# Kernel tuning notes

Hardware: AMD Instinct MI355X
Metric: run time of the kernel (lower is better)

## Reference

```python
import jax, jax.numpy as jnp
import numpy as np

N_NEIGHBORS = 5
N_TRAIN = 65536
N_TEST = 4096
DIM = 512
N_CLASSES = 10


def setup_inputs() -> dict:
    key = jax.random.key(0)
    k1, k2, k3 = jax.random.split(key, 3)
    X_train = jax.random.normal(k1, (N_TRAIN, DIM), dtype=jnp.float32)
    X_test = jax.random.normal(k2, (N_TEST, DIM), dtype=jnp.float32)
    y_train = jax.random.randint(k3, (N_TRAIN,), 0, N_CLASSES, dtype=jnp.int64)
    return {"X_train": X_train, "X_test": X_test, "y_train": y_train}


def _knn_predict(X_train, X_test, y_train, k):
    # Euclidean distances via the expanded form (GEMM-dominated):
    # ||t - x||^2 = ||t||^2 + ||x||^2 - 2 t.x
    t2 = jnp.sum(X_test * X_test, axis=-1, keepdims=True)          # [Nt, 1]
    x2 = jnp.sum(X_train * X_train, axis=-1)                        # [Ntr]
    cross = X_test @ X_train.T                                      # [Nt, Ntr]
    d2 = jnp.maximum(t2 + x2[None, :] - 2.0 * cross, 0.0)
    distances = jnp.sqrt(d2)                                        # cdist p=2

    # k smallest distances -> neighbor indices
    _, indices = jax.lax.top_k(-distances, k)                       # [Nt, k]
    nearest = y_train[indices]                                      # [Nt, k]

    counts = jnp.sum(nearest[:, :, None] == nearest[:, None, :], axis=-1)  # [Nt,k,k]->[Nt,k]
    max_c = jnp.max(counts, axis=-1, keepdims=True)
    big = jnp.iinfo(nearest.dtype).max
    candidates = jnp.where(counts == max_c, nearest, big)
    predictions = jnp.min(candidates, axis=-1)                      # [Nt]
    return predictions


def reference(X_train, X_test, y_train):
    return _knn_predict(X_train, X_test, y_train, N_NEIGHBORS)
```

## Files before the change

kernel.cpp:

```cpp
#include <hip/hip_runtime.h>
#include <cstdint>

#define N_TRAIN 65536
#define N_TEST  4096
#define DIM     512
#define K_NN    5
#define NSEG    32
#define SEG     (N_TRAIN / NSEG)

#define GTM 128
#define GTN 128
#define GBK 128
#define NCAND (NSEG * K_NN)
#define NRES  24
#define NSTEP ((SEG / GTN) * (DIM / GBK))
#define KMASK 0xFFFFF800u

typedef float f32x4  __attribute__((ext_vector_type(4)));
typedef float f32x16 __attribute__((ext_vector_type(16)));
typedef int   i32x8  __attribute__((ext_vector_type(8)));

#define GLDS16(g, l)                                                          \
    __builtin_amdgcn_global_load_lds(                                         \
        (__attribute__((address_space(1))) void*)(g),                         \
        (__attribute__((address_space(3))) void*)(l), 16, 0, 0)

__device__ inline unsigned f2e4m3_sw(float x) {
    float ax = fabsf(x);
    unsigned sgn = (__float_as_uint(x) >> 31) << 7;
    if (ax != ax) return sgn | 0x7Fu;
    if (ax >= 448.0f) return sgn | 0x7Eu;
    int ebits = (int)((__float_as_uint(ax) >> 23) & 0xFF);
    int e = ebits - 127;
    int shift = (e < -6 ? -6 : e) - 3;
    float q = exp2f((float)shift);
    float r = rintf(ax / q) * q;
    if (r >= 448.0f) return sgn | 0x7Eu;
    if (r == 0.0f) return sgn;
    unsigned ru = __float_as_uint(r);
    int re = (int)((ru >> 23) & 0xFF) - 127;
    if (re < -6) {
        unsigned k = (unsigned)(r * 512.0f);
        return sgn | k;
    }
    unsigned rm = (ru >> 20) & 0x7u;
    return sgn | ((unsigned)(re + 7) << 3) | rm;
}

__device__ inline unsigned pk4_fp8(float x0, float x1, float x2, float x3) {
#if __has_builtin(__builtin_amdgcn_cvt_pk_fp8_f32)
    unsigned r = (unsigned)__builtin_amdgcn_cvt_pk_fp8_f32(x0, x1, 0, 0);
    r = (unsigned)__builtin_amdgcn_cvt_pk_fp8_f32(x2, x3, (int)r, 1);
    return r;
#else
    return f2e4m3_sw(x0) | (f2e4m3_sw(x1) << 8) |
           (f2e4m3_sw(x2) << 16) | (f2e4m3_sw(x3) << 24);
#endif
}

__global__ __launch_bounds__(256) void cvtnorm8_k(const float* __restrict__ in,
                                                  unsigned char* __restrict__ outb,
                                                  float* __restrict__ outn,
                                                  int nrows) {
    int row  = blockIdx.x * 4 + (threadIdx.x >> 6);
    int lane = threadIdx.x & 63;
    if (row >= nrows) return;
    const float4* p = (const float4*)(in + (size_t)row * DIM) + lane * 2;
    float4 a = p[0], b = p[1];
    float s = a.x*a.x + a.y*a.y + a.z*a.z + a.w*a.w
            + b.x*b.x + b.y*b.y + b.z*b.z + b.w*b.w;
    uint2 v;
    v.x = pk4_fp8(a.x, a.y, a.z, a.w);
    v.y = pk4_fp8(b.x, b.y, b.z, b.w);
    *((uint2*)(outb + (size_t)row * DIM) + lane) = v;
#pragma unroll
    for (int off = 32; off > 0; off >>= 1) s += __shfl_xor(s, off, 64);
    if (lane == 0) outn[row] = s;
}

__global__ __launch_bounds__(256) void norms_k(const float* __restrict__ X,
                                               float* __restrict__ out,
                                               int nrows) {
    int row  = blockIdx.x * 4 + (threadIdx.x >> 6);
    int lane = threadIdx.x & 63;
    if (row >= nrows) return;
    const float4* xp = (const float4*)(X + (size_t)row * DIM);
    float4 a = xp[lane];
    float4 b = xp[lane + 64];
    float s = a.x*a.x + a.y*a.y + a.z*a.z + a.w*a.w
            + b.x*b.x + b.y*b.y + b.z*b.z + b.w*b.w;
#pragma unroll
    for (int off = 32; off > 0; off >>= 1) s += __shfl_down(s, off, 64);
    if (lane == 0) out[row] = s;
}

__device__ inline void ins5(unsigned long long key, unsigned long long* top) {
    if (key < top[4]) {
        unsigned long long k0 = top[0], k1 = top[1], k2 = top[2], k3 = top[3];
        top[0] = key < k0 ? key : k0;
        top[1] = key < k0 ? k0 : (key < k1 ? key : k1);
        top[2] = key < k1 ? k1 : (key < k2 ? key : k2);
        top[3] = key < k2 ? k2 : (key < k3 ? key : k3);
        top[4] = key < k3 ? k3 : key;
    }
}

__device__ inline void ins5u(unsigned key, unsigned* top) {
    if (key < top[4]) {
        unsigned k0 = top[0], k1 = top[1], k2 = top[2], k3 = top[3];
        top[0] = key < k0 ? key : k0;
        top[1] = key < k0 ? k0 : (key < k1 ? key : k1);
        top[2] = key < k1 ? k1 : (key < k2 ? key : k2);
        top[3] = key < k2 ? k2 : (key < k3 ? key : k3);
        top[4] = key < k3 ? k3 : key;
    }
}

__device__ inline unsigned fmono(float v) {
    unsigned u = __float_as_uint(v);
    return (u & 0x80000000u) ? ~u : (u | 0x80000000u);
}

#if __has_builtin(__builtin_amdgcn_mfma_scale_f32_32x32x64_f8f6f4)
__global__ __launch_bounds__(256, 2) void knn_mfma_k(
    const unsigned char* __restrict__ Xtr8,
    const unsigned char* __restrict__ Xte8,
    const float* __restrict__ x2,
    unsigned* __restrict__ cand)
{
    __shared__ __align__(16) unsigned char As[2][GTM * GBK];
    __shared__ __align__(16) unsigned char Bs[2][GTN * GBK];

    const int t    = threadIdx.x;
    const int lane = t & 63;
    const int w    = t >> 6;
    const int wr   = w >> 1, wc = w & 1;
    const int l31  = lane & 31;
    const int hi   = lane >> 5;
    const int r7   = lane & 7;
    const int row0 = blockIdx.x * GTM;
    const int seg0 = blockIdx.y * SEG;

    unsigned top5[2][K_NN];
#pragma unroll
    for (int nt = 0; nt < 2; ++nt)
#pragma unroll
        for (int p = 0; p < K_NN; ++p) top5[nt][p] = 0xFFFFFFFFu;

    int off[4];
#pragma unroll
    for (int j = 0; j < 4; ++j) {
        const int cs = j * 256 + t;
        const int gr = cs >> 3;
        off[j] = gr * DIM + (((cs ^ gr) & 7) << 4);
    }

    auto stage = [&](int s, int b) {
        const int k0 = (s & 3) * GBK;
        const unsigned char* ab = Xte8 + (size_t)row0 * DIM + k0;
        const unsigned char* bb = Xtr8 + (size_t)(seg0 + (s >> 2) * GTN) * DIM + k0;
#pragma unroll
        for (int j = 0; j < 4; ++j) {
            const int ldsb = (j * 256 + w * 64) * 16;
            GLDS16(ab + off[j], &As[b][ldsb]);
            GLDS16(bb + off[j], &Bs[b][ldsb]);
        }
    };

    stage(0, 0);
    __syncthreads();

#pragma unroll 1
    for (int ct = 0; ct < SEG / GTN; ++ct) {
        const int col0 = seg0 + ct * GTN;
        f32x16 acc[2][2];
#pragma unroll
        for (int mt = 0; mt < 2; ++mt)
#pragma unroll
            for (int nt = 0; nt < 2; ++nt)
#pragma unroll
                for (int e = 0; e < 16; ++e) acc[mt][nt][e] = 0.f;

#pragma unroll 1
        for (int kk = 0; kk < DIM / GBK; ++kk) {
            const int s = ct * (DIM / GBK) + kk;
            if (s + 1 < NSTEP) stage(s + 1, (kk + 1) & 1);

            const unsigned char* Ab = As[kk & 1];
            const unsigned char* Bb = Bs[kk & 1];
#pragma unroll
            for (int ks = 0; ks < 2; ++ks) {
                const int xq = (ks * 64 + hi * 32) ^ (r7 << 4);
                i32x8 trf[2], tef[2];
#pragma unroll
                for (int mt = 0; mt < 2; ++mt) {
                    const unsigned char* p = &Bb[(wr * 64 + mt * 32 + l31) * GBK];
                    int4 lo = *(const int4*)&p[xq];
                    int4 hx = *(const int4*)&p[xq ^ 16];
                    trf[mt] = (i32x8){lo.x, lo.y, lo.z, lo.w, hx.x, hx.y, hx.z, hx.w};
                }
#pragma unroll
                for (int nt = 0; nt < 2; ++nt) {
                    const unsigned char* p = &Ab[(wc * 64 + nt * 32 + l31) * GBK];
                    int4 lo = *(const int4*)&p[xq];
                    int4 hx = *(const int4*)&p[xq ^ 16];
                    tef[nt] = (i32x8){lo.x, lo.y, lo.z, lo.w, hx.x, hx.y, hx.z, hx.w};
                }
#pragma unroll
                for (int mt = 0; mt < 2; ++mt)
#pragma unroll
                    for (int nt = 0; nt < 2; ++nt)
                        acc[mt][nt] = __builtin_amdgcn_mfma_scale_f32_32x32x64_f8f6f4(
                            trf[mt], tef[nt], acc[mt][nt],
                            0 , 0 ,
                            0, 0x7F7F7F7F, 0, 0x7F7F7F7F );
            }
            __syncthreads();
        }

        f32x4 x2r[2][4];
#pragma unroll
        for (int mt = 0; mt < 2; ++mt)
#pragma unroll
            for (int g = 0; g < 4; ++g)
                x2r[mt][g] = *(const f32x4*)&x2[col0 + wr * 64 + mt * 32 + g * 8 + 4 * hi];

        const int cbase = ct * GTN + wr * 64;
#pragma unroll
        for (int nt = 0; nt < 2; ++nt) {
            float dv[2][16];
            float gm[2][4];
#pragma unroll
            for (int mt = 0; mt < 2; ++mt)
#pragma unroll
                for (int g = 0; g < 4; ++g) {
#pragma unroll
                    for (int i = 0; i < 4; ++i)
                        dv[mt][g * 4 + i] =
                            fmaf(-2.f, acc[mt][nt][g * 4 + i], x2r[mt][g][i]);
                    gm[mt][g] = fminf(fminf(dv[mt][g*4+0], dv[mt][g*4+1]),
                                      fminf(dv[mt][g*4+2], dv[mt][g*4+3]));
                }
            float dmin = fminf(
                fminf(fminf(gm[0][0], gm[0][1]), fminf(gm[0][2], gm[0][3])),
                fminf(fminf(gm[1][0], gm[1][1]), fminf(gm[1][2], gm[1][3])));
            if ((fmono(dmin) & KMASK) <= top5[nt][4]) {
#pragma unroll
                for (int mt = 0; mt < 2; ++mt)
#pragma unroll
                    for (int g = 0; g < 4; ++g) {
                        if ((fmono(gm[mt][g]) & KMASK) <= top5[nt][4]) {
#pragma unroll
                            for (int i = 0; i < 4; ++i) {
                                unsigned key = (fmono(dv[mt][g * 4 + i]) & KMASK)
                                    | (unsigned)(cbase + mt * 32 + g * 8 + 4 * hi + i);
                                ins5u(key, top5[nt]);
                            }
                        }
                    }
            }
        }
    }

    __syncthreads();
    unsigned* MB = (unsigned*)&As[0][0];
#pragma unroll
    for (int nt = 0; nt < 2; ++nt)
#pragma unroll
        for (int p = 0; p < K_NN; ++p) MB[t * 10 + nt * K_NN + p] = top5[nt][p];
    __syncthreads();

    if (t < GTM) {
        const int r   = t;
        const int mwc = r >> 6, mnt = (r >> 5) & 1, mn5 = r & 31;
        unsigned tp[K_NN];
#pragma unroll
        for (int p = 0; p < K_NN; ++p) tp[p] = 0xFFFFFFFFu;
#pragma unroll
        for (int w2 = 0; w2 < 2; ++w2)
#pragma unroll
            for (int h2 = 0; h2 < 2; ++h2) {
                const int tid = (w2 * 2 + mwc) * 64 + h2 * 32 + mn5;
                const unsigned* src = &MB[tid * 10 + mnt * K_NN];
#pragma unroll
                for (int p = 0; p < K_NN; ++p) ins5u(src[p], tp);
            }
        unsigned* cr = cand + (size_t)(row0 + r) * NCAND + blockIdx.y * K_NN;
#pragma unroll
        for (int p = 0; p < K_NN; ++p) cr[p] = tp[p];
    }
}

#else
#if __has_builtin(__builtin_amdgcn_mfma_scale_f32_16x16x128_f8f6f4)
__device__ inline f32x4 mfma_k128(i32x8 a, i32x8 b, f32x4 c) {
    return __builtin_amdgcn_mfma_scale_f32_16x16x128_f8f6f4(
        a, b, c, 0, 0, 0, 0x7F7F7F7F, 0, 0x7F7F7F7F);
}
#else
__device__ inline long long mk64(int lo, int hi) {
    return (long long)(((unsigned long long)(unsigned)hi << 32) | (unsigned)lo);
}
__device__ inline f32x4 mfma_k128(i32x8 a, i32x8 b, f32x4 c) {
    c = __builtin_amdgcn_mfma_f32_16x16x32_fp8_fp8(mk64(a[0],a[1]), mk64(b[0],b[1]), c, 0,0,0);
    c = __builtin_amdgcn_mfma_f32_16x16x32_fp8_fp8(mk64(a[2],a[3]), mk64(b[2],b[3]), c, 0,0,0);
    c = __builtin_amdgcn_mfma_f32_16x16x32_fp8_fp8(mk64(a[4],a[5]), mk64(b[4],b[5]), c, 0,0,0);
    c = __builtin_amdgcn_mfma_f32_16x16x32_fp8_fp8(mk64(a[6],a[7]), mk64(b[6],b[7]), c, 0,0,0);
    return c;
}
#endif

__global__ __launch_bounds__(256, 2) void knn_mfma_k(
    const unsigned char* __restrict__ Xtr8,
    const unsigned char* __restrict__ Xte8,
    const float* __restrict__ x2,
    unsigned* __restrict__ cand)
{
    __shared__ __align__(16) unsigned char As[2][GTM * GBK];
    __shared__ __align__(16) unsigned char Bs[2][GTN * GBK];

    const int t     = threadIdx.x;
    const int lane  = t & 63;
    const int w     = t >> 6;
    const int wr    = w >> 1, wc = w & 1;
    const int col_l = lane & 15, quad = lane >> 4;
    const int row0  = blockIdx.x * GTM;
    const int seg0  = blockIdx.y * SEG;

    unsigned top5[4][K_NN];
#pragma unroll
    for (int nt = 0; nt < 4; ++nt)
#pragma unroll
        for (int p = 0; p < K_NN; ++p) top5[nt][p] = 0xFFFFFFFFu;

    int off[4];
#pragma unroll
    for (int j = 0; j < 4; ++j) {
        const int cs = j * 256 + t;
        const int gr = cs >> 3;
        off[j] = gr * DIM + (((cs ^ gr) & 7) << 4);
    }

    auto stage = [&](int s, int b) {
        const int k0 = (s & 3) * GBK;
        const unsigned char* ab = Xte8 + (size_t)row0 * DIM + k0;
        const unsigned char* bb = Xtr8 + (size_t)(seg0 + (s >> 2) * GTN) * DIM + k0;
#pragma unroll
        for (int j = 0; j < 4; ++j) {
            const int ldsb = (j * 256 + w * 64) * 16;
            GLDS16(ab + off[j], &As[b][ldsb]);
            GLDS16(bb + off[j], &Bs[b][ldsb]);
        }
    };

    stage(0, 0);
    __syncthreads();

    const int xq = (quad * 32) ^ ((lane & 7) << 4);

#pragma unroll 1
    for (int ct = 0; ct < SEG / GTN; ++ct) {
        const int col0 = seg0 + ct * GTN;
        f32x4 acc[4][4];
#pragma unroll
        for (int mt = 0; mt < 4; ++mt)
#pragma unroll
            for (int nt = 0; nt < 4; ++nt)
                acc[mt][nt] = (f32x4){0.f, 0.f, 0.f, 0.f};

        f32x4 x2r[4];
#pragma unroll
        for (int mt = 0; mt < 4; ++mt)
            x2r[mt] = *(const f32x4*)&x2[col0 + wr * 64 + mt * 16 + quad * 4];

#pragma unroll 1
        for (int kk = 0; kk < DIM / GBK; ++kk) {
            const int s = ct * (DIM / GBK) + kk;
            if (s + 1 < NSTEP) stage(s + 1, (kk + 1) & 1);

            const unsigned char* Ab = As[kk & 1];
            const unsigned char* Bb = Bs[kk & 1];
            i32x8 trf[4], tef[4];
#pragma unroll
            for (int mt = 0; mt < 4; ++mt) {
                const unsigned char* p = &Bb[(wr * 64 + mt * 16 + col_l) * GBK];
                int4 lo = *(const int4*)&p[xq];
                int4 hx = *(const int4*)&p[xq ^ 16];
                trf[mt] = (i32x8){lo.x, lo.y, lo.z, lo.w, hx.x, hx.y, hx.z, hx.w};
            }
#pragma unroll
            for (int nt = 0; nt < 4; ++nt) {
                const unsigned char* p = &Ab[(wc * 64 + nt * 16 + col_l) * GBK];
                int4 lo = *(const int4*)&p[xq];
                int4 hx = *(const int4*)&p[xq ^ 16];
                tef[nt] = (i32x8){lo.x, lo.y, lo.z, lo.w, hx.x, hx.y, hx.z, hx.w};
            }
#pragma unroll
            for (int mt = 0; mt < 4; ++mt)
#pragma unroll
                for (int nt = 0; nt < 4; ++nt)
                    acc[mt][nt] = mfma_k128(trf[mt], tef[nt], acc[mt][nt]);

            __syncthreads();
        }

        const int cb = ct * GTN + wr * 64 + quad * 4;
#pragma unroll
        for (int nt = 0; nt < 4; ++nt) {
            float dv[16];
            float dmin = __builtin_inff();
#pragma unroll
            for (int mt = 0; mt < 4; ++mt) {
                f32x4 a = acc[mt][nt];
                dv[mt * 4 + 0] = fmaf(-2.f, a.x, x2r[mt].x);
                dv[mt * 4 + 1] = fmaf(-2.f, a.y, x2r[mt].y);
                dv[mt * 4 + 2] = fmaf(-2.f, a.z, x2r[mt].z);
                dv[mt * 4 + 3] = fmaf(-2.f, a.w, x2r[mt].w);
                float g = fminf(fminf(dv[mt*4+0], dv[mt*4+1]),
                                fminf(dv[mt*4+2], dv[mt*4+3]));
                dmin = fminf(dmin, g);
            }
            if ((fmono(dmin) & KMASK) <= top5[nt][4]) {
#pragma unroll
                for (int mt = 0; mt < 4; ++mt) {
                    float g = fminf(fminf(dv[mt*4+0], dv[mt*4+1]),
                                    fminf(dv[mt*4+2], dv[mt*4+3]));
                    if ((fmono(g) & KMASK) <= top5[nt][4]) {
#pragma unroll
                        for (int i = 0; i < 4; ++i) {
                            unsigned key = (fmono(dv[mt * 4 + i]) & KMASK)
                                         | (unsigned)(cb + mt * 16 + i);
                            ins5u(key, top5[nt]);
                        }
                    }
                }
            }
        }
    }

    __syncthreads();
    unsigned* MB = (unsigned*)&As[0][0];
#pragma unroll
    for (int nt = 0; nt < 4; ++nt)
#pragma unroll
        for (int p = 0; p < K_NN; ++p) MB[t * 20 + nt * K_NN + p] = top5[nt][p];
    __syncthreads();

    if (t < GTM) {
        const int r   = t;
        const int mwc = r >> 6, mnt = (r >> 4) & 3, mcl = r & 15;
        unsigned tp[K_NN];
#pragma unroll
        for (int p = 0; p < K_NN; ++p) tp[p] = 0xFFFFFFFFu;
#pragma unroll
        for (int w2 = 0; w2 < 2; ++w2)
#pragma unroll
            for (int q = 0; q < 4; ++q) {
                const int tid = (w2 * 2 + mwc) * 64 + q * 16 + mcl;
                const unsigned* src = &MB[tid * 20 + mnt * K_NN];
#pragma unroll
                for (int p = 0; p < K_NN; ++p) ins5u(src[p], tp);
            }
        unsigned* cr = cand + (size_t)(row0 + r) * NCAND + blockIdx.y * K_NN;
#pragma unroll
        for (int p = 0; p < K_NN; ++p) cr[p] = tp[p];
    }
}
#endif

__global__ __launch_bounds__(256) void rescore_vote_k(
    const float* __restrict__ Xtr, const float* __restrict__ Xte,
    const float* __restrict__ x2,  const float* __restrict__ t2,
    const unsigned* __restrict__ cand,
    const int* __restrict__ y, int* __restrict__ out)
{
    int row  = blockIdx.x * 4 + (threadIdx.x >> 6);
    int lane = threadIdx.x & 63;
    const unsigned* cr = cand + (size_t)row * NCAND;

    auto expand = [](unsigned k, int e) -> unsigned long long {
        unsigned gcol = (unsigned)(e / K_NN) * SEG + (k & 0x7FFu);
        return ((unsigned long long)k << 32) | gcol;
    };
    unsigned long long c0 = expand(cr[lane], lane);
    unsigned long long c1 = expand(cr[64 + lane], 64 + lane);
    unsigned long long c2 = (lane < NCAND - 128)
                          ? expand(cr[128 + lane], 128 + lane) : ~0ull;

    unsigned cols[NRES];
#pragma unroll 1
    for (int i = 0; i < NRES; ++i) {
        unsigned long long m = c0 < c1 ? c0 : c1;
        m = c2 < m ? c2 : m;
#pragma unroll
        for (int off = 32; off > 0; off >>= 1) {
            unsigned long long o = __shfl_xor(m, off, 64);
            m = o < m ? o : m;
        }
        cols[i] = (unsigned)(m & 0xffffffffu);
        if (c0 == m) c0 = ~0ull;
        if (c1 == m) c1 = ~0ull;
        if (c2 == m) c2 = ~0ull;
    }

    const float4* te = (const float4*)(Xte + (size_t)row * DIM);
    float4 e0 = te[lane * 2], e1 = te[lane * 2 + 1];
    float t2r = t2[row];
    float d2s[NRES];
#pragma unroll 4
    for (int i = 0; i < NRES; ++i) {
        const float4* tr = (const float4*)(Xtr + (size_t)cols[i] * DIM);
        float4 p = tr[lane * 2], q = tr[lane * 2 + 1];
        float s = e0.x * p.x;
        s = fmaf(e0.y, p.y, s); s = fmaf(e0.z, p.z, s); s = fmaf(e0.w, p.w, s);
        s = fmaf(e1.x, q.x, s); s = fmaf(e1.y, q.y, s);
        s = fmaf(e1.z, q.z, s); s = fmaf(e1.w, q.w, s);
#pragma unroll
        for (int off = 32; off > 0; off >>= 1) s += __shfl_xor(s, off, 64);
        d2s[i] = fmaxf(t2r + x2[cols[i]] - 2.0f * s, 0.0f);
    }

    unsigned long long top[K_NN];
#pragma unroll
    for (int p = 0; p < K_NN; ++p) top[p] = ~0ull;
#pragma unroll
    for (int i = 0; i < NRES; ++i)
        ins5(((unsigned long long)__float_as_uint(d2s[i]) << 32) | cols[i], top);

    if (lane == 0) {
        int labs[K_NN];
#pragma unroll
        for (int p = 0; p < K_NN; ++p) labs[p] = y[(unsigned)(top[p] & 0xffffffffu)];
        int bestLab = 0x7fffffff, bestCnt = 0;
#pragma unroll
        for (int p = 0; p < K_NN; ++p) {
            int cnt = 0;
#pragma unroll
            for (int q = 0; q < K_NN; ++q) cnt += (labs[q] == labs[p]) ? 1 : 0;
            if (cnt > bestCnt || (cnt == bestCnt && labs[p] < bestLab)) {
                bestCnt = cnt; bestLab = labs[p];
            }
        }
        out[row] = bestLab;
    }
}

#define FTM 64
#define FTN 128
#define FBK 16
#define FSEG (N_TRAIN / 8)

__global__ __launch_bounds__(256) void knn_tile_k(
    const float* __restrict__ Xtr, const float* __restrict__ Xte,
    const float* __restrict__ x2,  const float* __restrict__ t2,
    unsigned long long* __restrict__ cand)
{
    __shared__ float As[FBK][FTM];
    __shared__ float Bs[FBK][FTN];
    __shared__ unsigned long long MB[FTM][16 * K_NN];

    const int t   = threadIdx.x;
    const int ty  = t >> 4;
    const int tx  = t & 15;
    const int row0 = blockIdx.x * FTM;
    const int seg0 = blockIdx.y * FSEG;

    float t2r[4];
#pragma unroll
    for (int j = 0; j < 4; ++j) t2r[j] = t2[row0 + ty * 4 + j];

    unsigned long long top[4][K_NN];
#pragma unroll
    for (int j = 0; j < 4; ++j)
#pragma unroll
        for (int p = 0; p < K_NN; ++p) top[j][p] = ~0ull;

    const int srow = t >> 2;
    const int skq  = (t & 3) * 4;

    for (int ct = 0; ct < FSEG / FTN; ++ct) {
        const int col0 = seg0 + ct * FTN;
        float acc[4][8] = {};

        for (int k0 = 0; k0 < DIM; k0 += FBK) {
            float4 av  = *(const float4*)(Xte + (size_t)(row0 + srow) * DIM + k0 + skq);
            float4 bv0 = *(const float4*)(Xtr + (size_t)(col0 + srow) * DIM + k0 + skq);
            float4 bv1 = *(const float4*)(Xtr + (size_t)(col0 + 64 + srow) * DIM + k0 + skq);
            __syncthreads();
            As[skq + 0][srow] = av.x;  As[skq + 1][srow] = av.y;
            As[skq + 2][srow] = av.z;  As[skq + 3][srow] = av.w;
            Bs[skq + 0][srow] = bv0.x; Bs[skq + 1][srow] = bv0.y;
            Bs[skq + 2][srow] = bv0.z; Bs[skq + 3][srow] = bv0.w;
            Bs[skq + 0][srow + 64] = bv1.x; Bs[skq + 1][srow + 64] = bv1.y;
            Bs[skq + 2][srow + 64] = bv1.z; Bs[skq + 3][srow + 64] = bv1.w;
            __syncthreads();

#pragma unroll
            for (int k = 0; k < FBK; ++k) {
                float4 a  = *(const float4*)&As[k][ty * 4];
                float4 b0 = *(const float4*)&Bs[k][tx * 8];
                float4 b1 = *(const float4*)&Bs[k][tx * 8 + 4];
                float a4[4] = {a.x, a.y, a.z, a.w};
                float b8[8] = {b0.x, b0.y, b0.z, b0.w, b1.x, b1.y, b1.z, b1.w};
#pragma unroll
                for (int j = 0; j < 4; ++j)
#pragma unroll
                    for (int l = 0; l < 8; ++l)
                        acc[j][l] = fmaf(a4[j], b8[l], acc[j][l]);
            }
        }

#pragma unroll
        for (int j = 0; j < 4; ++j) {
#pragma unroll
            for (int l = 0; l < 8; ++l) {
                int col = col0 + tx * 8 + l;
                float d2 = fmaxf(t2r[j] + x2[col] - 2.0f * acc[j][l], 0.0f);
                unsigned long long key =
                    ((unsigned long long)__float_as_uint(d2) << 32) | (unsigned)col;
                ins5(key, top[j]);
            }
        }
    }

#pragma unroll
    for (int j = 0; j < 4; ++j)
#pragma unroll
        for (int p = 0; p < K_NN; ++p)
            MB[ty * 4 + j][tx * K_NN + p] = top[j][p];
    __syncthreads();

    if (t < FTM) {
        unsigned long long last = 0;
        for (int p = 0; p < K_NN; ++p) {
            unsigned long long best = ~0ull;
            for (int q = 0; q < 16 * K_NN; ++q) {
                unsigned long long v = MB[t][q];
                if (v > last && v < best) best = v;
            }
            cand[(size_t)(row0 + t) * 40 + blockIdx.y * K_NN + p] = best;
            last = best;
        }
    }
}

__global__ __launch_bounds__(256) void knn_final_k(
    const unsigned long long* __restrict__ cand,
    const int* __restrict__ y, int* __restrict__ out)
{
    int r = blockIdx.x * 256 + threadIdx.x;
    if (r >= N_TEST) return;
    const unsigned long long* c = cand + (size_t)r * 40;

    unsigned long long top[K_NN];
#pragma unroll
    for (int p = 0; p < K_NN; ++p) top[p] = ~0ull;
#pragma unroll
    for (int i = 0; i < 40; ++i) ins5(c[i], top);

    int labs[K_NN];
#pragma unroll
    for (int p = 0; p < K_NN; ++p) labs[p] = y[(unsigned)(top[p] & 0xffffffffu)];

    int bestLab = 0x7fffffff, bestCnt = 0;
#pragma unroll
    for (int p = 0; p < K_NN; ++p) {
        int cnt = 0;
#pragma unroll
        for (int q = 0; q < K_NN; ++q) cnt += (labs[q] == labs[p]) ? 1 : 0;
        if (cnt > bestCnt || (cnt == bestCnt && labs[p] < bestLab)) {
            bestCnt = cnt; bestLab = labs[p];
        }
    }
    out[r] = bestLab;
}

extern "C" void kernel_launch(void* const* d_in, const int* in_sizes, int n_in,
                              void* d_out, int out_size, void* d_ws, size_t ws_size,
                              hipStream_t stream) {
    const float* Xtr = (const float*)d_in[0];
    const float* Xte = (const float*)d_in[1];
    const int*   y   = (const int*)d_in[2];
    int* out = (int*)d_out;

    char* ws = (char*)d_ws;
    float* x2 = (float*)ws;
    float* t2 = (float*)(ws + 262144);

    const size_t NEED = 74448896;

    if (ws_size >= NEED) {
        unsigned* cand = (unsigned*)(ws + 278528);
        unsigned char* Xte8 = (unsigned char*)(ws + 3145728);
        unsigned char* Xtr8 = (unsigned char*)(ws + 7340032);

        cvtnorm8_k<<<N_TRAIN / 4, 256, 0, stream>>>(Xtr, Xtr8, x2, N_TRAIN);
        cvtnorm8_k<<<N_TEST / 4, 256, 0, stream>>>(Xte, Xte8, t2, N_TEST);

        knn_mfma_k<<<dim3(N_TEST / GTM, NSEG), 256, 0, stream>>>(Xtr8, Xte8, x2, cand);
        rescore_vote_k<<<N_TEST / 4, 256, 0, stream>>>(Xtr, Xte, x2, t2, cand, y, out);
    } else {
        unsigned long long* cand = (unsigned long long*)(ws + 278528);
        norms_k<<<N_TRAIN / 4, 256, 0, stream>>>(Xtr, x2, N_TRAIN);
        norms_k<<<N_TEST / 4, 256, 0, stream>>>(Xte, t2, N_TEST);
        knn_tile_k<<<dim3(N_TEST / FTM, 8), 256, 0, stream>>>(Xtr, Xte, x2, t2, cand);
        knn_final_k<<<N_TEST / 256, 256, 0, stream>>>(cand, y, out);
    }
}
```

Measured before the change: 520.7 us.

## Keep full test tile resident in LDS and triple-buffer train tiles

Loads the whole 128x512 FP8 test tile into shared memory once, so only train tiles are streamed. Train tiles are triple-buffered with explicit vmcnt waits and a single barrier per step, and the K and column-tile loops are flattened into one loop with the epilogue run every fourth step. This removes redundant reloading of the test tile and should overlap loads with MFMA better. LDS use rises to about 112KB, so launch bounds drop to one block per SM, which reduces occupancy and may expose epilogue latency.

```diff
diff --git a/kernel.cpp b/kernel.cpp
--- a/kernel.cpp
+++ b/kernel.cpp
@@ -122,14 +122,14 @@
 }
 
 #if __has_builtin(__builtin_amdgcn_mfma_scale_f32_32x32x64_f8f6f4)
-__global__ __launch_bounds__(256, 2) void knn_mfma_k(
+__global__ __launch_bounds__(256, 1) void knn_mfma_k(
     const unsigned char* __restrict__ Xtr8,
     const unsigned char* __restrict__ Xte8,
     const float* __restrict__ x2,
     unsigned* __restrict__ cand)
 {
-    __shared__ __align__(16) unsigned char As[2][GTM * GBK];
-    __shared__ __align__(16) unsigned char Bs[2][GTN * GBK];
+    __shared__ __align__(16) unsigned char As[GTM * DIM];
+    __shared__ __align__(16) unsigned char Bs[3][GTN * GBK];
 
     const int t    = threadIdx.x;
     const int lane = t & 63;
@@ -147,6 +147,15 @@
 #pragma unroll
         for (int p = 0; p < K_NN; ++p) top5[nt][p] = 0xFFFFFFFFu;
 
+#pragma unroll
+    for (int j = 0; j < 16; ++j) {
+        const int cs = j * 256 + t;
+        const int gr = cs >> 5;
+        const int ss = (cs & 24) | ((cs ^ gr) & 7);
+        GLDS16(Xte8 + (size_t)(row0 + gr) * DIM + (ss << 4),
+               &As[(j * 256 + w * 64) * 16]);
+    }
+
     int off[4];
 #pragma unroll
     for (int j = 0; j < 4; ++j) {
@@ -155,76 +164,34 @@
         off[j] = gr * DIM + (((cs ^ gr) & 7) << 4);
     }
 
-    auto stage = [&](int s, int b) {
+    auto stageT = [&](int s, int b) {
         const int k0 = (s & 3) * GBK;
-        const unsigned char* ab = Xte8 + (size_t)row0 * DIM + k0;
         const unsigned char* bb = Xtr8 + (size_t)(seg0 + (s >> 2) * GTN) * DIM + k0;
 #pragma unroll
         for (int j = 0; j < 4; ++j) {
             const int ldsb = (j * 256 + w * 64) * 16;
-            GLDS16(ab + off[j], &As[b][ldsb]);
             GLDS16(bb + off[j], &Bs[b][ldsb]);
         }
     };
 
-    stage(0, 0);
-    __syncthreads();
-
-#pragma unroll 1
-    for (int ct = 0; ct < SEG / GTN; ++ct) {
+    f32x16 acc[2][2];
+    auto zero_acc = [&]() {
+#pragma unroll
+        for (int mt = 0; mt < 2; ++mt)
+#pragma unroll
+            for (int nt = 0; nt < 2; ++nt)
+#pragma unroll
+                for (int e = 0; e < 16; ++e) acc[mt][nt][e] = 0.f;
+    };
+
+    auto epilogue = [&](int ct) {
         const int col0 = seg0 + ct * GTN;
-        f32x16 acc[2][2];
-#pragma unroll
-        for (int mt = 0; mt < 2; ++mt)
-#pragma unroll
-            for (int nt = 0; nt < 2; ++nt)
-#pragma unroll
-                for (int e = 0; e < 16; ++e) acc[mt][nt][e] = 0.f;
-
-#pragma unroll 1
-        for (int kk = 0; kk < DIM / GBK; ++kk) {
-            const int s = ct * (DIM / GBK) + kk;
-            if (s + 1 < NSTEP) stage(s + 1, (kk + 1) & 1);
-
-            const unsigned char* Ab = As[kk & 1];
-            const unsigned char* Bb = Bs[kk & 1];
-#pragma unroll
-            for (int ks = 0; ks < 2; ++ks) {
-                const int xq = (ks * 64 + hi * 32) ^ (r7 << 4);
-                i32x8 trf[2], tef[2];
-#pragma unroll
-                for (int mt = 0; mt < 2; ++mt) {
-                    const unsigned char* p = &Bb[(wr * 64 + mt * 32 + l31) * GBK];
-                    int4 lo = *(const int4*)&p[xq];
-                    int4 hx = *(const int4*)&p[xq ^ 16];
-                    trf[mt] = (i32x8){lo.x, lo.y, lo.z, lo.w, hx.x, hx.y, hx.z, hx.w};
-                }
-#pragma unroll
-                for (int nt = 0; nt < 2; ++nt) {
-                    const unsigned char* p = &Ab[(wc * 64 + nt * 32 + l31) * GBK];
-                    int4 lo = *(const int4*)&p[xq];
-                    int4 hx = *(const int4*)&p[xq ^ 16];
-                    tef[nt] = (i32x8){lo.x, lo.y, lo.z, lo.w, hx.x, hx.y, hx.z, hx.w};
-                }
-#pragma unroll
-                for (int mt = 0; mt < 2; ++mt)
-#pragma unroll
-                    for (int nt = 0; nt < 2; ++nt)
-                        acc[mt][nt] = __builtin_amdgcn_mfma_scale_f32_32x32x64_f8f6f4(
-                            trf[mt], tef[nt], acc[mt][nt],
-                            0 , 0 ,
-                            0, 0x7F7F7F7F, 0, 0x7F7F7F7F );
-            }
-            __syncthreads();
-        }
-
         f32x4 x2r[2][4];
 #pragma unroll
         for (int mt = 0; mt < 2; ++mt)
 #pragma unroll
             for (int g = 0; g < 4; ++g)
                 x2r[mt][g] = *(const f32x4*)&x2[col0 + wr * 64 + mt * 32 + g * 8 + 4 * hi];
-
         const int cbase = ct * GTN + wr * 64;
 #pragma unroll
         for (int nt = 0; nt < 2; ++nt) {
@@ -260,10 +227,62 @@
                     }
             }
         }
-    }
-
+    };
+
+    stageT(0, 0);
+    stageT(1, 1);
     __syncthreads();
-    unsigned* MB = (unsigned*)&As[0][0];
+
+    zero_acc();
+
+#pragma unroll 1
+    for (int s = 0; s < NSTEP; ++s) {
+        if (s < NSTEP - 1) {
+            asm volatile("s_waitcnt vmcnt(4)" ::: "memory");
+        } else {
+            asm volatile("s_waitcnt vmcnt(0)" ::: "memory");
+        }
+        __builtin_amdgcn_s_barrier();
+        if (s + 2 < NSTEP) stageT(s + 2, (s + 2) % 3);
+
+        const unsigned char* Bb = Bs[s % 3];
+        const int kkb = (s & 3) * GBK;
+#pragma unroll
+        for (int ks = 0; ks < 2; ++ks) {
+            const int xq = (ks * 64 + hi * 32) ^ (r7 << 4);
+            i32x8 trf[2], tef[2];
+#pragma unroll
+            for (int mt = 0; mt < 2; ++mt) {
+                const unsigned char* p = &Bb[(wr * 64 + mt * 32 + l31) * GBK];
+                int4 lo = *(const int4*)&p[xq];
+                int4 hx = *(const int4*)&p[xq ^ 16];
+                trf[mt] = (i32x8){lo.x, lo.y, lo.z, lo.w, hx.x, hx.y, hx.z, hx.w};
+            }
+#pragma unroll
+            for (int nt = 0; nt < 2; ++nt) {
+                const unsigned char* p = &As[(wc * 64 + nt * 32 + l31) * DIM + kkb];
+                int4 lo = *(const int4*)&p[xq];
+                int4 hx = *(const int4*)&p[xq ^ 16];
+                tef[nt] = (i32x8){lo.x, lo.y, lo.z, lo.w, hx.x, hx.y, hx.z, hx.w};
+            }
+#pragma unroll
+            for (int mt = 0; mt < 2; ++mt)
+#pragma unroll
+                for (int nt = 0; nt < 2; ++nt)
+                    acc[mt][nt] = __builtin_amdgcn_mfma_scale_f32_32x32x64_f8f6f4(
+                        trf[mt], tef[nt], acc[mt][nt],
+                        0 , 0 ,
+                        0, 0x7F7F7F7F, 0, 0x7F7F7F7F );
+        }
+
+        if ((s & 3) == 3) {
+            epilogue(s >> 2);
+            zero_acc();
+        }
+    }
+
+    __syncthreads();
+    unsigned* MB = (unsigned*)&Bs[0][0];
 #pragma unroll
     for (int nt = 0; nt < 2; ++nt)
 #pragma unroll
```

Result: slower. 808.1 us (+55.2%).
